# Kernel optimization log

Hardware: AMD Instinct MI355X
Metric: run time of the kernel (lower is better)

## Reference

```python
import jax, jax.numpy as jnp
import numpy as np

ALPHA = 0.2  # leaky relu negative slope (LinearNet default)


def _init_linear(key, fan_in, fan_out):
    kw, kb = jax.random.split(key)
    lim = 1.0 / np.sqrt(fan_in)
    W = jax.random.uniform(kw, (fan_in, fan_out), jnp.float32, -lim, lim)
    b = jax.random.uniform(kb, (fan_out,), jnp.float32, -lim, lim)
    return W, b


def setup_inputs() -> dict:
    key = jax.random.key(0)
    keys = jax.random.split(key, 8)
    B, N, F = 8, 512, 32
    x = jax.random.normal(keys[0], (B, N, F), jnp.float32)
    # fe: [2F=64 -> 64 -> 64 -> 64], all layers leaky-relu (final_linear=False)
    fe_W0, fe_b0 = _init_linear(keys[1], 2 * F, 64)
    fe_W1, fe_b1 = _init_linear(keys[2], 64, 64)
    fe_W2, fe_b2 = _init_linear(keys[3], 64, 64)
    # fn: [64 + F = 96 -> 128 -> 128 -> 32], last layer linear (final_linear=True)
    fn_W0, fn_b0 = _init_linear(keys[4], 64 + F, 128)
    fn_W1, fn_b1 = _init_linear(keys[5], 128, 128)
    fn_W2, fn_b2 = _init_linear(keys[6], 128, 32)
    return {
        "x": x,
        "fe_W0": fe_W0, "fe_b0": fe_b0,
        "fe_W1": fe_W1, "fe_b1": fe_b1,
        "fe_W2": fe_W2, "fe_b2": fe_b2,
        "fn_W0": fn_W0, "fn_b0": fn_b0,
        "fn_W1": fn_W1, "fn_b1": fn_b1,
        "fn_W2": fn_W2, "fn_b2": fn_b2,
    }


def reference(x, fe_W0, fe_b0, fe_W1, fe_b1, fe_W2, fe_b2,
              fn_W0, fn_b0, fn_W1, fn_b1, fn_W2, fn_b2):
    B, N, F = x.shape
    # all-pairs edge inputs: A[b,i,j] = concat(x[b,i], x[b,j])  (x1=repeat rows, x2=tile)
    xi = jnp.broadcast_to(x[:, :, None, :], (B, N, N, F))
    xj = jnp.broadcast_to(x[:, None, :, :], (B, N, N, F))
    A = jnp.concatenate([xi, xj], axis=-1)  # [B, N, N, 2F]
    # edge MLP fe: leaky relu after every layer (final_linear=False)
    for W, b in ((fe_W0, fe_b0), (fe_W1, fe_b1), (fe_W2, fe_b2)):
        A = jax.nn.leaky_relu(A @ W + b, negative_slope=ALPHA)
    # sum aggregation over the sender axis j
    agg = jnp.sum(A, axis=2)  # [B, N, K]
    h = jnp.concatenate([agg, x], axis=-1)  # [B, N, K + F]
    # node MLP fn: leaky relu on hidden layers, final layer linear
    h = jax.nn.leaky_relu(h @ fn_W0 + fn_b0, negative_slope=ALPHA)
    h = jax.nn.leaky_relu(h @ fn_W1 + fn_b1, negative_slope=ALPHA)
    out = h @ fn_W2 + fn_b2  # [B, N, output_node_size]
    return out
```

## Files before the change

### kernel.cpp

```cpp
#include <hip/hip_runtime.h>
#include <hip/hip_bf16.h>

#define ALPHA 0.2f
static __device__ __forceinline__ float lrel(float x) { return fmaxf(x, ALPHA * x); }

typedef __attribute__((ext_vector_type(8))) short bf16x8;
typedef __attribute__((ext_vector_type(4))) float f32x4;

union FragU { bf16x8 v; unsigned int u[4]; uint4 q; };

static __device__ __forceinline__ unsigned int pk2(float a, float b) {
    unsigned int r;
    asm("v_cvt_pk_bf16_f32 %0, %1, %2" : "=v"(r) : "v"(a), "v"(b));
    return r;
}
static __device__ __forceinline__ unsigned int cvl2(float a, float b) {
    return pk2(lrel(a), lrel(b));
}
static __device__ __forceinline__ unsigned short f2bf(float x) {
    union { float f; unsigned int u; } c;
    c.f = x;
    unsigned int r = c.u + 0x7FFFu + ((c.u >> 16) & 1u);
    return (unsigned short)(r >> 16);
}
static __device__ __forceinline__ int pi64(int s) {
    return 32 * ((s >> 4) >> 1) + 8 * ((s >> 2) & 3) + 4 * ((s >> 4) & 1) + (s & 3);
}

__global__ __launch_bounds__(256) void k_uv(
    const float* __restrict__ x, const float* __restrict__ W0, const float* __restrict__ b0,
    const float* __restrict__ W1, const float* __restrict__ W2,
    float* __restrict__ Upi, unsigned short* __restrict__ xbf, unsigned int* __restrict__ WF)
{
    if (blockIdx.x == 1024) {
        const int t = threadIdx.x;
        const int l = t & 63, part = t >> 6;
        const int lo = l & 15, g = l >> 4;
        for (int ff = part; ff < 20; ff += 4) {
            unsigned int o[4];
            if (ff < 4) {
                const int nf = ff;
                const int pc = 32 * (nf >> 1) + 8 * (lo >> 2) + 4 * (nf & 1) + (lo & 3);
#pragma unroll
                for (int uq = 0; uq < 4; ++uq) {
                    const int k0 = 8 * g + 2 * uq;
                    o[uq] = pk2(W0[(32 + k0) * 64 + pc], W0[(33 + k0) * 64 + pc]);
                }
            } else if (ff < 12) {
                const int s = (ff - 4) >> 2, nf = (ff - 4) & 3;
                const int pc = 32 * (nf >> 1) + 8 * (lo >> 2) + 4 * (nf & 1) + (lo & 3);
#pragma unroll
                for (int uq = 0; uq < 4; ++uq) {
                    const int k0 = 32 * s + 8 * g + 2 * uq;
                    o[uq] = pk2(W1[k0 * 64 + pc], W1[(k0 + 1) * 64 + pc]);
                }
            } else {
                const int s = (ff - 12) >> 2, nf = (ff - 12) & 3;
                const int c2 = 16 * nf + lo;
#pragma unroll
                for (int uq = 0; uq < 4; ++uq) {
                    const int k0 = 32 * s + 8 * g + 2 * uq;
                    o[uq] = pk2(W2[k0 * 64 + c2], W2[(k0 + 1) * 64 + c2]);
                }
            }
            *(uint4*)(WF + (ff * 64 + l) * 4) = make_uint4(o[0], o[1], o[2], o[3]);
        }
        return;
    }
    const int idx = blockIdx.x * 256 + threadIdx.x;
    const int n = idx >> 6;
    const int slot = idx & 63;
    const int f = pi64(slot);
    const float* xr = x + n * 32;
    float u = b0[f];
#pragma unroll
    for (int i = 0; i < 32; ++i) u += xr[i] * W0[i * 64 + f];
    Upi[idx] = u;
    if (slot < 32) xbf[n * 32 + slot] = f2bf(xr[slot]);
}

__global__ __launch_bounds__(256, 2) void k_edge(
    const float* __restrict__ Upi, const unsigned short* __restrict__ xbf,
    const unsigned int* __restrict__ WF,
    const float* __restrict__ b1, const float* __restrict__ b2,
    float* __restrict__ AGG)
{
    __shared__ uint4 wlds[1024];
    const int tid = threadIdx.x;
    const int w = tid >> 6, l = tid & 63;
    const int lo = l & 15, g = l >> 4;
    const int bid = blockIdx.x;
    const int b = bid >> 7, ig = bid & 127;
    const int node = b * 512 + ig * 4 + w;

    for (int idx = tid; idx < 1024; idx += 256)
        wlds[idx] = ((const uint4*)WF)[256 + idx];

    FragU w0f[4];
    const uint4* wp = (const uint4*)WF;
#pragma unroll
    for (int nf = 0; nf < 4; ++nf) w0f[nf].q = wp[nf * 64 + l];

    f32x4 u0f[4], b1f[4], b2f[4];
#pragma unroll
    for (int nf = 0; nf < 4; ++nf) {
        const float4 t0 = *(const float4*)(Upi + node * 64 + nf * 16 + 4 * g);
        u0f[nf] = (f32x4){t0.x, t0.y, t0.z, t0.w};
        const float4 t1 = *(const float4*)(b1 + 32 * (nf >> 1) + 8 * g + 4 * (nf & 1));
        const float4 t2 = *(const float4*)(b2 + 16 * nf + 4 * g);
        b1f[nf] = (f32x4){t1.x, t1.y, t1.z, t1.w};
        b2f[nf] = (f32x4){t2.x, t2.y, t2.z, t2.w};
    }

    const unsigned short* xb = xbf + b * 512 * 32;

    FragU xjT0, xjB;
    xjT0.q = *(const uint4*)(xb + lo * 32 + 8 * g);
    xjB.q  = *(const uint4*)(xb + (16 + lo) * 32 + 8 * g);

    __syncthreads();

    f32x4 acc0p[4], acc1p[4], acc2p[4];
#pragma unroll
    for (int nf = 0; nf < 4; ++nf)
        acc0p[nf] = __builtin_amdgcn_mfma_f32_16x16x32_bf16(w0f[nf].v, xjT0.v, u0f[nf], 0, 0, 0);
#pragma unroll
    for (int nf = 0; nf < 4; ++nf) {
        f32x4 z = {0.f, 0.f, 0.f, 0.f};
        acc1p[nf] = z; acc2p[nf] = z;
    }

    float aggL[4][4];
#pragma unroll
    for (int nf = 0; nf < 4; ++nf)
#pragma unroll
        for (int r = 0; r < 4; ++r) aggL[nf][r] = 0.f;

#pragma unroll 2
    for (int k = 0; k < 34; ++k) {
        int widx = 0;
        asm volatile("" : "+v"(widx));

        const int jn = ((k + 2) & 31) * 16;
        FragU xjn;
        xjn.q = *(const uint4*)(xb + (jn + lo) * 32 + 8 * g);

        FragU q0, q1;
        q0.u[0] = cvl2(acc0p[0][0], acc0p[0][1]);
        q0.u[1] = cvl2(acc0p[0][2], acc0p[0][3]);
        q0.u[2] = cvl2(acc0p[1][0], acc0p[1][1]);
        q0.u[3] = cvl2(acc0p[1][2], acc0p[1][3]);
        q1.u[0] = cvl2(acc0p[2][0], acc0p[2][1]);
        q1.u[1] = cvl2(acc0p[2][2], acc0p[2][3]);
        q1.u[2] = cvl2(acc0p[3][0], acc0p[3][1]);
        q1.u[3] = cvl2(acc0p[3][2], acc0p[3][3]);

        f32x4 acc0n[4];
#pragma unroll
        for (int nf = 0; nf < 4; ++nf)
            acc0n[nf] = __builtin_amdgcn_mfma_f32_16x16x32_bf16(w0f[nf].v, xjB.v, u0f[nf], 0, 0, 0);

        FragU p0, p1;
        p0.u[0] = cvl2(acc1p[0][0], acc1p[0][1]);
        p0.u[1] = cvl2(acc1p[0][2], acc1p[0][3]);
        p0.u[2] = cvl2(acc1p[1][0], acc1p[1][1]);
        p0.u[3] = cvl2(acc1p[1][2], acc1p[1][3]);
        p1.u[0] = cvl2(acc1p[2][0], acc1p[2][1]);
        p1.u[1] = cvl2(acc1p[2][2], acc1p[2][3]);
        p1.u[2] = cvl2(acc1p[3][0], acc1p[3][1]);
        p1.u[3] = cvl2(acc1p[3][2], acc1p[3][3]);

        f32x4 acc1n[4];
#pragma unroll
        for (int nf = 0; nf < 4; ++nf) {
            FragU wa, wb;
            wa.q = wlds[widx + nf * 64 + l];
            wb.q = wlds[widx + (4 + nf) * 64 + l];
            acc1n[nf] = __builtin_amdgcn_mfma_f32_16x16x32_bf16(wa.v, q0.v, b1f[nf], 0, 0, 0);
            acc1n[nf] = __builtin_amdgcn_mfma_f32_16x16x32_bf16(wb.v, q1.v, acc1n[nf], 0, 0, 0);
        }

        if (k >= 2) {
#pragma unroll
            for (int nf = 0; nf < 4; ++nf)
#pragma unroll
                for (int r = 0; r < 4; ++r) aggL[nf][r] += lrel(acc2p[nf][r]);
        }

        f32x4 acc2n[4];
#pragma unroll
        for (int nf = 0; nf < 4; ++nf) {
            FragU wa, wb;
            wa.q = wlds[widx + (8 + nf) * 64 + l];
            wb.q = wlds[widx + (12 + nf) * 64 + l];
            acc2n[nf] = __builtin_amdgcn_mfma_f32_16x16x32_bf16(wa.v, p0.v, b2f[nf], 0, 0, 0);
            acc2n[nf] = __builtin_amdgcn_mfma_f32_16x16x32_bf16(wb.v, p1.v, acc2n[nf], 0, 0, 0);
        }

#pragma unroll
        for (int nf = 0; nf < 4; ++nf) {
            acc0p[nf] = acc0n[nf];
            acc1p[nf] = acc1n[nf];
            acc2p[nf] = acc2n[nf];
        }
        xjB = xjn;
    }

#pragma unroll
    for (int nf = 0; nf < 4; ++nf)
#pragma unroll
        for (int r = 0; r < 4; ++r) {
            float v = aggL[nf][r];
            v += __shfl_xor(v, 1);
            v += __shfl_xor(v, 2);
            v += __shfl_xor(v, 4);
            v += __shfl_xor(v, 8);
            aggL[nf][r] = v;
        }
    if (lo == 0) {
#pragma unroll
        for (int nf = 0; nf < 4; ++nf) {
            float4 o = {aggL[nf][0], aggL[nf][1], aggL[nf][2], aggL[nf][3]};
            *(float4*)(AGG + node * 64 + 16 * nf + 4 * g) = o;
        }
    }
}

__global__ __launch_bounds__(256) void k_fn(
    const float* __restrict__ AGG, const float* __restrict__ x,
    const float* __restrict__ W0, const float* __restrict__ b0,
    const float* __restrict__ W1, const float* __restrict__ b1,
    const float* __restrict__ W2, const float* __restrict__ b2,
    float* __restrict__ out)
{
    __shared__ float in96T[96][8];
    __shared__ float h1T[128][8];
    __shared__ float h2T[128][8];
    const int t = threadIdx.x;
    const int half = t >> 7, f = t & 127;
    const int node0 = blockIdx.x * 8;

    for (int idx = t; idx < 768; idx += 256) {
        int nn = idx & 7, k = idx >> 3;
        in96T[k][nn] = (k < 64) ? AGG[(node0 + nn) * 64 + k]
                                : x[(node0 + nn) * 32 + (k - 64)];
    }
    __syncthreads();

    {
        float a0 = b0[f], a1 = a0, a2 = a0, a3 = a0;
#pragma unroll 4
        for (int k = 0; k < 96; ++k) {
            const float4 iv = *(const float4*)(&in96T[k][4 * half]);
            const float wv = W0[k * 128 + f];
            a0 += iv.x * wv; a1 += iv.y * wv; a2 += iv.z * wv; a3 += iv.w * wv;
        }
        float4 o = {lrel(a0), lrel(a1), lrel(a2), lrel(a3)};
        *(float4*)(&h1T[f][4 * half]) = o;
    }
    __syncthreads();

    {
        float a0 = b1[f], a1 = a0, a2 = a0, a3 = a0;
#pragma unroll 4
        for (int k = 0; k < 128; ++k) {
            const float4 iv = *(const float4*)(&h1T[k][4 * half]);
            const float wv = W1[k * 128 + f];
            a0 += iv.x * wv; a1 += iv.y * wv; a2 += iv.z * wv; a3 += iv.w * wv;
        }
        float4 o = {lrel(a0), lrel(a1), lrel(a2), lrel(a3)};
        *(float4*)(&h2T[f][4 * half]) = o;
    }
    __syncthreads();

    {
        const int nn = t >> 5, fo = t & 31;
        float a = b2[fo];
#pragma unroll 4
        for (int k = 0; k < 128; ++k) a += h2T[k][nn] * W2[k * 32 + fo];
        out[(node0 + nn) * 32 + fo] = a;
    }
}

extern "C" void kernel_launch(void* const* d_in, const int* in_sizes, int n_in,
                              void* d_out, int out_size, void* d_ws, size_t ws_size,
                              hipStream_t stream)
{
    const float* x    = (const float*)d_in[0];
    const float* feW0 = (const float*)d_in[1];
    const float* feb0 = (const float*)d_in[2];
    const float* feW1 = (const float*)d_in[3];
    const float* feb1 = (const float*)d_in[4];
    const float* feW2 = (const float*)d_in[5];
    const float* feb2 = (const float*)d_in[6];
    const float* fnW0 = (const float*)d_in[7];
    const float* fnb0 = (const float*)d_in[8];
    const float* fnW1 = (const float*)d_in[9];
    const float* fnb1 = (const float*)d_in[10];
    const float* fnW2 = (const float*)d_in[11];
    const float* fnb2 = (const float*)d_in[12];
    float* out = (float*)d_out;

    float* Upi = (float*)d_ws;
    float* AGG = Upi + 262144;
    unsigned short* xbf = (unsigned short*)(AGG + 262144);
    unsigned int* WF = (unsigned int*)(xbf + 131072);

    hipLaunchKernelGGL(k_uv,   dim3(1025), dim3(256), 0, stream, x, feW0, feb0, feW1, feW2, Upi, xbf, WF);
    hipLaunchKernelGGL(k_edge, dim3(1024), dim3(256), 0, stream, Upi, xbf, WF, feb1, feb2, AGG);
    hipLaunchKernelGGL(k_fn,   dim3(512),  dim3(256), 0, stream, AGG, x, fnW0, fnb0, fnW1, fnb1, fnW2, fnb2, out);
}
```

Before: 85.27 us.

## Ping-pong MFMA and VALU phases across two wave groups with barriers

The edge kernel now runs 512-thread blocks of 8 waves split into two groups of 4. The groups alternate between a matrix phase (all three layers' MFMAs, at raised priority) and a vector phase (bf16 packing, leaky-relu, aggregation), separated by block barriers, so the MFMA and VALU units are kept busy by different waves. The leaky-relu accumulate is rewritten as two FMAs using an abs term, and the MFMAs are issued through inline asm. The cost is a block barrier on every half-step and half as many blocks, and relying on asm-pinned MFMAs risks scheduling hazards.

```diff
diff --git a/kernel.cpp b/kernel.cpp
--- a/kernel.cpp
+++ b/kernel.cpp
@@ -8,6 +8,15 @@
 typedef __attribute__((ext_vector_type(4))) float f32x4;
 
 union FragU { bf16x8 v; unsigned int u[4]; uint4 q; };
+
+static __device__ __forceinline__ f32x4 mfma_init(bf16x8 a, bf16x8 b, f32x4 c) {
+    f32x4 d;
+    asm("v_mfma_f32_16x16x32_bf16 %0, %1, %2, %3" : "=&v"(d) : "v"(a), "v"(b), "v"(c));
+    return d;
+}
+static __device__ __forceinline__ void mfma_acc(f32x4& acc, bf16x8 a, bf16x8 b) {
+    asm("v_mfma_f32_16x16x32_bf16 %0, %1, %2, %0" : "+v"(acc) : "v"(a), "v"(b));
+}
 
 static __device__ __forceinline__ unsigned int pk2(float a, float b) {
     unsigned int r;
@@ -16,6 +25,9 @@
 }
 static __device__ __forceinline__ unsigned int cvl2(float a, float b) {
     return pk2(lrel(a), lrel(b));
+}
+static __device__ __forceinline__ void aggfma(float& agg, float x) {
+    agg = fmaf(0.6f, x, fmaf(0.4f, fabsf(x), agg));
 }
 static __device__ __forceinline__ unsigned short f2bf(float x) {
     union { float f; unsigned int u; } c;
@@ -79,7 +91,7 @@
     if (slot < 32) xbf[n * 32 + slot] = f2bf(xr[slot]);
 }
 
-__global__ __launch_bounds__(256, 2) void k_edge(
+__global__ __launch_bounds__(512, 2) void k_edge(
     const float* __restrict__ Upi, const unsigned short* __restrict__ xbf,
     const unsigned int* __restrict__ WF,
     const float* __restrict__ b1, const float* __restrict__ b2,
@@ -87,13 +99,14 @@
 {
     __shared__ uint4 wlds[1024];
     const int tid = threadIdx.x;
-    const int w = tid >> 6, l = tid & 63;
+    const int wave = tid >> 6, l = tid & 63;
+    const int grp = wave >> 2;
     const int lo = l & 15, g = l >> 4;
     const int bid = blockIdx.x;
-    const int b = bid >> 7, ig = bid & 127;
-    const int node = b * 512 + ig * 4 + w;
-
-    for (int idx = tid; idx < 1024; idx += 256)
+    const int b = bid >> 6, ig = bid & 63;
+    const int node = b * 512 + ig * 8 + wave;
+
+    for (int idx = tid; idx < 1024; idx += 512)
         wlds[idx] = ((const uint4*)WF)[256 + idx];
 
     FragU w0f[4];
@@ -114,97 +127,85 @@
 
     const unsigned short* xb = xbf + b * 512 * 32;
 
-    FragU xjT0, xjB;
-    xjT0.q = *(const uint4*)(xb + lo * 32 + 8 * g);
-    xjB.q  = *(const uint4*)(xb + (16 + lo) * 32 + 8 * g);
-
-    __syncthreads();
-
-    f32x4 acc0p[4], acc1p[4], acc2p[4];
-#pragma unroll
-    for (int nf = 0; nf < 4; ++nf)
-        acc0p[nf] = __builtin_amdgcn_mfma_f32_16x16x32_bf16(w0f[nf].v, xjT0.v, u0f[nf], 0, 0, 0);
+    FragU xjc, xjn, q0z, q1z, p0z, p1z;
+    xjc.q = *(const uint4*)(xb + lo * 32 + 8 * g);
+    xjn.q = *(const uint4*)(xb + (16 + lo) * 32 + 8 * g);
+    f32x4 A0[4], A1[4], A2[4];
 #pragma unroll
     for (int nf = 0; nf < 4; ++nf) {
         f32x4 z = {0.f, 0.f, 0.f, 0.f};
-        acc1p[nf] = z; acc2p[nf] = z;
-    }
-
+        A0[nf] = z; A1[nf] = z; A2[nf] = z;
+        q0z.u[nf] = 0u; q1z.u[nf] = 0u; p0z.u[nf] = 0u; p1z.u[nf] = 0u;
+    }
     float aggL[4][4];
 #pragma unroll
     for (int nf = 0; nf < 4; ++nf)
 #pragma unroll
         for (int r = 0; r < 4; ++r) aggL[nf][r] = 0.f;
 
-#pragma unroll 2
-    for (int k = 0; k < 34; ++k) {
+    __syncthreads();
+
+    auto MPH = [&]() {
         int widx = 0;
         asm volatile("" : "+v"(widx));
-
-        const int jn = ((k + 2) & 31) * 16;
-        FragU xjn;
-        xjn.q = *(const uint4*)(xb + (jn + lo) * 32 + 8 * g);
-
-        FragU q0, q1;
-        q0.u[0] = cvl2(acc0p[0][0], acc0p[0][1]);
-        q0.u[1] = cvl2(acc0p[0][2], acc0p[0][3]);
-        q0.u[2] = cvl2(acc0p[1][0], acc0p[1][1]);
-        q0.u[3] = cvl2(acc0p[1][2], acc0p[1][3]);
-        q1.u[0] = cvl2(acc0p[2][0], acc0p[2][1]);
-        q1.u[1] = cvl2(acc0p[2][2], acc0p[2][3]);
-        q1.u[2] = cvl2(acc0p[3][0], acc0p[3][1]);
-        q1.u[3] = cvl2(acc0p[3][2], acc0p[3][3]);
-
-        f32x4 acc0n[4];
+        __builtin_amdgcn_s_setprio(1);
 #pragma unroll
         for (int nf = 0; nf < 4; ++nf)
-            acc0n[nf] = __builtin_amdgcn_mfma_f32_16x16x32_bf16(w0f[nf].v, xjB.v, u0f[nf], 0, 0, 0);
-
-        FragU p0, p1;
-        p0.u[0] = cvl2(acc1p[0][0], acc1p[0][1]);
-        p0.u[1] = cvl2(acc1p[0][2], acc1p[0][3]);
-        p0.u[2] = cvl2(acc1p[1][0], acc1p[1][1]);
-        p0.u[3] = cvl2(acc1p[1][2], acc1p[1][3]);
-        p1.u[0] = cvl2(acc1p[2][0], acc1p[2][1]);
-        p1.u[1] = cvl2(acc1p[2][2], acc1p[2][3]);
-        p1.u[2] = cvl2(acc1p[3][0], acc1p[3][1]);
-        p1.u[3] = cvl2(acc1p[3][2], acc1p[3][3]);
-
-        f32x4 acc1n[4];
+            A0[nf] = mfma_init(w0f[nf].v, xjc.v, u0f[nf]);
 #pragma unroll
         for (int nf = 0; nf < 4; ++nf) {
             FragU wa, wb;
             wa.q = wlds[widx + nf * 64 + l];
             wb.q = wlds[widx + (4 + nf) * 64 + l];
-            acc1n[nf] = __builtin_amdgcn_mfma_f32_16x16x32_bf16(wa.v, q0.v, b1f[nf], 0, 0, 0);
-            acc1n[nf] = __builtin_amdgcn_mfma_f32_16x16x32_bf16(wb.v, q1.v, acc1n[nf], 0, 0, 0);
-        }
-
-        if (k >= 2) {
-#pragma unroll
-            for (int nf = 0; nf < 4; ++nf)
-#pragma unroll
-                for (int r = 0; r < 4; ++r) aggL[nf][r] += lrel(acc2p[nf][r]);
-        }
-
-        f32x4 acc2n[4];
+            A1[nf] = mfma_init(wa.v, q0z.v, b1f[nf]);
+            mfma_acc(A1[nf], wb.v, q1z.v);
+        }
 #pragma unroll
         for (int nf = 0; nf < 4; ++nf) {
             FragU wa, wb;
             wa.q = wlds[widx + (8 + nf) * 64 + l];
             wb.q = wlds[widx + (12 + nf) * 64 + l];
-            acc2n[nf] = __builtin_amdgcn_mfma_f32_16x16x32_bf16(wa.v, p0.v, b2f[nf], 0, 0, 0);
-            acc2n[nf] = __builtin_amdgcn_mfma_f32_16x16x32_bf16(wb.v, p1.v, acc2n[nf], 0, 0, 0);
-        }
-
-#pragma unroll
-        for (int nf = 0; nf < 4; ++nf) {
-            acc0p[nf] = acc0n[nf];
-            acc1p[nf] = acc1n[nf];
-            acc2p[nf] = acc2n[nf];
-        }
-        xjB = xjn;
-    }
+            A2[nf] = mfma_init(wa.v, p0z.v, b2f[nf]);
+            mfma_acc(A2[nf], wb.v, p1z.v);
+        }
+        __builtin_amdgcn_s_setprio(0);
+        xjc = xjn;
+    };
+    auto VPH = [&](int kk) {
+        const int jn = ((kk + 2) & 31) * 16;
+        xjn.q = *(const uint4*)(xb + (jn + lo) * 32 + 8 * g);
+        q0z.u[0] = cvl2(A0[0][0], A0[0][1]);
+        q0z.u[1] = cvl2(A0[0][2], A0[0][3]);
+        q0z.u[2] = cvl2(A0[1][0], A0[1][1]);
+        q0z.u[3] = cvl2(A0[1][2], A0[1][3]);
+        q1z.u[0] = cvl2(A0[2][0], A0[2][1]);
+        q1z.u[1] = cvl2(A0[2][2], A0[2][3]);
+        q1z.u[2] = cvl2(A0[3][0], A0[3][1]);
+        q1z.u[3] = cvl2(A0[3][2], A0[3][3]);
+        p0z.u[0] = cvl2(A1[0][0], A1[0][1]);
+        p0z.u[1] = cvl2(A1[0][2], A1[0][3]);
+        p0z.u[2] = cvl2(A1[1][0], A1[1][1]);
+        p0z.u[3] = cvl2(A1[1][2], A1[1][3]);
+        p1z.u[0] = cvl2(A1[2][0], A1[2][1]);
+        p1z.u[1] = cvl2(A1[2][2], A1[2][3]);
+        p1z.u[2] = cvl2(A1[3][0], A1[3][1]);
+        p1z.u[3] = cvl2(A1[3][2], A1[3][3]);
+        if (kk >= 2) {
+#pragma unroll
+            for (int nf = 0; nf < 4; ++nf)
+#pragma unroll
+                for (int r = 0; r < 4; ++r) aggfma(aggL[nf][r], A2[nf][r]);
+        }
+    };
+
+#pragma unroll 1
+    for (int k = 0; k < 34; ++k) {
+        if (grp == 0) MPH(); else VPH(k - 1);
+        __builtin_amdgcn_s_barrier();
+        if (grp == 0) VPH(k); else MPH();
+        __builtin_amdgcn_s_barrier();
+    }
+    if (grp == 1) VPH(33);
 
 #pragma unroll
     for (int nf = 0; nf < 4; ++nf)
@@ -307,6 +308,6 @@
     unsigned int* WF = (unsigned int*)(xbf + 131072);
 
     hipLaunchKernelGGL(k_uv,   dim3(1025), dim3(256), 0, stream, x, feW0, feb0, feW1, feW2, Upi, xbf, WF);
-    hipLaunchKernelGGL(k_edge, dim3(1024), dim3(256), 0, stream, Upi, xbf, WF, feb1, feb2, AGG);
+    hipLaunchKernelGGL(k_edge, dim3(512),  dim3(512), 0, stream, Upi, xbf, WF, feb1, feb2, AGG);
     hipLaunchKernelGGL(k_fn,   dim3(512),  dim3(256), 0, stream, AGG, x, fnW0, fnb0, fnW1, fnb1, fnW2, fnb2, out);
 }
```

Result: slower. 87.68 us (+2.8%).
